# Kernel tuning notes

Measured on AMD Instinct MI355X. Metric: run time of the kernel, lower is better.

Reference implementation:

```python
import jax, jax.numpy as jnp
import numpy as np

B, N, C_IN, C_OUT, K = 2, 8192, 128, 128, 21  # K = num_neighbors + 1 (self)
EPS = 1e-5

def knn_idx(xyz, k):
    # xyz: [B,N,3] -> idx [B,N,k] of k nearest neighbors (self included)
    d2 = jnp.sum(xyz * xyz, axis=-1)  # [B,N]
    dist = d2[:, :, None] + d2[:, None, :] - 2.0 * jnp.einsum('bnd,bmd->bnm', xyz, xyz)
    _, idx = jax.lax.top_k(-dist, k)
    return idx

def group_points(pts, idx):
    # pts [B,N,D], idx [B,N,K] -> [B,N,K,D]
    return jax.vmap(lambda p, i: p[i])(pts, idx)

def group_feats(f, idx):
    # f [B,C,N], idx [B,N,K] -> [B,C,N,K]
    return jax.vmap(lambda ff, i: ff[:, i])(f, idx)

def conv_bn_relu(x, W, g, b, m, v):
    # 1x1 conv (bias=False) + BatchNorm (inference stats) + ReLU
    y = jnp.einsum('oc,bcnk->bonk', W, x)
    inv = g / jnp.sqrt(v + EPS)
    return jax.nn.relu(y * inv[None, :, None, None] + (b - m * inv)[None, :, None, None])

def setup_inputs():
    key = jax.random.key(0)
    ks = jax.random.split(key, 12)
    return {
        'xyz': jax.random.normal(ks[0], (B, N, 3), jnp.float32),
        'f': jax.random.normal(ks[1], (B, C_IN, N), jnp.float32),
        'W_geo': jax.random.normal(ks[2], (C_OUT, 6), jnp.float32) * 0.1,
        'g_geo': jax.random.uniform(ks[3], (C_OUT,), jnp.float32, 0.5, 1.5),
        'b_geo': jax.random.normal(ks[4], (C_OUT,), jnp.float32) * 0.1,
        'm_geo': jax.random.normal(ks[5], (C_OUT,), jnp.float32) * 0.1,
        'v_geo': jax.random.uniform(ks[6], (C_OUT,), jnp.float32, 0.5, 1.5),
        'W_feat': jax.random.normal(ks[7], (C_OUT, 2 * C_IN), jnp.float32) * 0.05,
        'g_feat': jax.random.uniform(ks[8], (C_OUT,), jnp.float32, 0.5, 1.5),
        'b_feat': jax.random.normal(ks[9], (C_OUT,), jnp.float32) * 0.1,
        'm_feat': jax.random.normal(ks[10], (C_OUT,), jnp.float32) * 0.1,
        'v_feat': jax.random.uniform(ks[11], (C_OUT,), jnp.float32, 0.5, 1.5),
    }

def reference(xyz, f, W_geo, g_geo, b_geo, m_geo, v_geo, W_feat, g_feat, b_feat, m_feat, v_feat):
    idx = knn_idx(xyz, K)                                   # [B,N,K]
    grouped_xyz = group_points(xyz, idx)                    # [B,N,K,3]
    xyz_diff = jnp.transpose(grouped_xyz - xyz[:, :, None, :], (0, 3, 1, 2))  # [B,3,N,K]
    center = jnp.broadcast_to(jnp.transpose(xyz, (0, 2, 1))[:, :, :, None], (B, 3, N, K))
    G_geo = jnp.concatenate([center, xyz_diff], axis=1)     # [B,6,N,K]
    grouped_f = group_feats(f, idx)                         # [B,C,N,K]
    center_f = jnp.broadcast_to(f[:, :, :, None], (B, C_IN, N, K))
    G_feat = jnp.concatenate([center_f, grouped_f - center_f], axis=1)  # [B,2C,N,K]
    G_geo = conv_bn_relu(G_geo, W_geo, g_geo, b_geo, m_geo, v_geo)      # [B,C_OUT,N,K]
    G_feat = conv_bn_relu(G_feat, W_feat, g_feat, b_feat, m_feat, v_feat)
    feature = jnp.concatenate([G_geo, G_feat], axis=1)      # [B,2*C_OUT,N,K]
    return jnp.max(feature, axis=-1)                        # [B,2*C_OUT,N]
```

## Files before the change

### kernel.cpp

```cpp
#include <hip/hip_runtime.h>

typedef unsigned int u32;
typedef unsigned long long u64;
typedef unsigned short u16;

#define DEV __device__ __forceinline__

DEV u16 f2bf(float x) {
  u32 u = __float_as_uint(x);
  u32 r = u + 0x7fffu + ((u >> 16) & 1u);
  return (u16)(r >> 16);
}
DEV float bflo(u32 d) { return __uint_as_float(d << 16); }
DEV float bfhi(u32 d) { return __uint_as_float(d & 0xffff0000u); }
DEV u64 sortable64(double f) {
  long long b = __double_as_longlong(f);
  return (u64)b ^ (u64)((b >> 63) | (long long)0x8000000000000000ll);
}
DEV double ddist(double qx, double qy, double qz, double qd2,
                 float mxf, float myf, float mzf) {
  double cx = (double)mxf, cy = (double)myf, cz = (double)mzf;
  double cd2 = cx * cx + cy * cy + cz * cz;
  double dot = cx * qx + cy * qy + cz * qz;
  return (qd2 + cd2) - 2.0 * dot;
}

#define NB 2
#define NN 8192
#define NC 128
#define KK 21
#define MARGIN 1e-3f

__global__ __launch_bounds__(1024) void k_knnprep(
    const float* __restrict__ xyz, int* __restrict__ knn,
    const float* __restrict__ Wf, const float* __restrict__ gf, const float* __restrict__ bf_,
    const float* __restrict__ mf, const float* __restrict__ vf,
    const float* __restrict__ Wg, const float* __restrict__ gg, const float* __restrict__ bg,
    const float* __restrict__ mg, const float* __restrict__ vg,
    u16* __restrict__ Wt, float* __restrict__ beta_f,
    float* __restrict__ Wgu, float* __restrict__ Wgv, float* __restrict__ beta_g) {
  __shared__ float4 sc[NN];
  __shared__ u16 ssurv[64][128];
  __shared__ u32 scnt[64];

  const int t = threadIdx.x;

  if (blockIdx.x < 32) {
    int g = (blockIdx.x << 10) + t;
    int c = g >> 8, o = g & 255;
    float val;
    if (o < 128) {
      float inv = gf[o] / sqrtf(vf[o] + 1e-5f);
      val = inv * (Wf[o * 256 + c] - Wf[o * 256 + c + 128]);
    } else {
      int o2 = o - 128;
      float inv = gf[o2] / sqrtf(vf[o2] + 1e-5f);
      val = inv * Wf[o2 * 256 + c + 128];
    }
    Wt[c * 256 + o] = f2bf(val);
    if (g < 128) {
      float inv = gf[g] / sqrtf(vf[g] + 1e-5f);
      beta_f[g] = bf_[g] - mf[g] * inv;
    } else if (g < 256) {
      int oo = g - 128;
      float invg = gg[oo] / sqrtf(vg[oo] + 1e-5f);
#pragma unroll
      for (int d = 0; d < 3; ++d) {
        Wgu[oo * 3 + d] = invg * (Wg[oo * 6 + d] - Wg[oo * 6 + 3 + d]);
        Wgv[oo * 3 + d] = invg * Wg[oo * 6 + 3 + d];
      }
      beta_g[oo] = bg[oo] - mg[oo] * invg;
    }
    return;
  }

  const int kb = blockIdx.x - 32;
  const int b = kb >> 7;
  const int n0 = (kb & 127) << 6;
  const float* X = xyz + b * (NN * 3);

  if (t < 64) scnt[t] = 0u;

  const int w = t >> 6, lane = t & 63;

  float mx[4], my[4], mz[4];
#pragma unroll
  for (int i = 0; i < 4; ++i) {
    int q = n0 + (w << 2) + i;
    mx[i] = -2.0f * X[q * 3];
    my[i] = -2.0f * X[q * 3 + 1];
    mz[i] = -2.0f * X[q * 3 + 2];
  }

#pragma unroll
  for (int k = 0; k < 8; ++k) {
    int c = (k << 10) + t;
    float x = X[c * 3], y = X[c * 3 + 1], z = X[c * 3 + 2];
    float d2 = __builtin_fmaf(x, x, __builtin_fmaf(y, y, z * z));
    sc[c] = make_float4(x, y, z, d2);
  }
  __syncthreads();

  float mn[4];
#pragma unroll
  for (int i = 0; i < 4; ++i) mn[i] = __builtin_inff();

#pragma unroll 4
  for (int cc = 0; cc < NN; cc += 64) {
    float4 C = sc[cc + lane];
#pragma unroll
    for (int i = 0; i < 4; ++i) {
      float s = __builtin_fmaf(C.x, mx[i],
                __builtin_fmaf(C.y, my[i],
                __builtin_fmaf(C.z, mz[i], C.w)));
      mn[i] = fminf(mn[i], s);
    }
  }

  float thr[4];
#pragma unroll
  for (int i = 0; i < 4; ++i) {
    float v = mn[i];
#pragma unroll
    for (int k = 2; k <= 64; k <<= 1) {
#pragma unroll
      for (int j = k >> 1; j > 0; j >>= 1) {
        float p = __shfl_xor(v, j);
        bool takeMin = (((lane & k) == 0) == ((lane & j) == 0));
        v = takeMin ? fminf(v, p) : fmaxf(v, p);
      }
    }
    thr[i] = __shfl(v, 20) + MARGIN;
  }

#pragma unroll 2
  for (int cc = 0; cc < NN; cc += 64) {
    float4 C = sc[cc + lane];
    int mbase = cc + lane;
#pragma unroll
    for (int i = 0; i < 4; ++i) {
      float s = __builtin_fmaf(C.x, mx[i],
                __builtin_fmaf(C.y, my[i],
                __builtin_fmaf(C.z, mz[i], C.w)));
      if (s <= thr[i]) {
        int qq = (w << 2) + i;
        u32 slot = atomicAdd(&scnt[qq], 1u);
        if (slot < 128u) ssurv[qq][slot] = (u16)mbase;
      }
    }
  }
  __syncthreads();

#pragma unroll 1
  for (int i = 0; i < 4; ++i) {
    const int qq = (w << 2) + i;
    const int q = n0 + qq;
    double Qx = (double)X[q * 3], Qy = (double)X[q * 3 + 1], Qz = (double)X[q * 3 + 2];
    double Qd2 = Qx * Qx + Qy * Qy + Qz * Qz;
    u32 cnt = scnt[qq];
    int* outp = knn + ((b << 13) + q) * KK;

    bool v0 = ((u32)lane < cnt);
    u32 m0 = v0 ? (u32)ssurv[qq][lane] : 0u;
    double s0 = ddist(Qx, Qy, Qz, Qd2, X[m0 * 3], X[m0 * 3 + 1], X[m0 * 3 + 2]);
    u64 k0 = v0 ? ((sortable64(s0) & 0xFFFFFFFFFFFFE000ull) | (u64)m0) : ~0ull;

    if (cnt <= 64u) {
      u64 v = k0;
#pragma unroll
      for (int k = 2; k <= 64; k <<= 1) {
#pragma unroll
        for (int j = k >> 1; j > 0; j >>= 1) {
          u64 p = __shfl_xor(v, j);
          bool takeMin = (((lane & k) == 0) == ((lane & j) == 0));
          bool pl = p < v;
          u64 mnv = pl ? p : v;
          u64 mxv = pl ? v : p;
          v = takeMin ? mnv : mxv;
        }
      }
      if (lane < KK) outp[lane] = (int)(v & 8191ull);
    } else {
      bool v1 = ((u32)(lane + 64) < cnt);
      u32 m1 = v1 ? (u32)ssurv[qq][lane + 64] : 0u;
      double s1 = ddist(Qx, Qy, Qz, Qd2, X[m1 * 3], X[m1 * 3 + 1], X[m1 * 3 + 2]);
      u64 k1 = v1 ? ((sortable64(s1) & 0xFFFFFFFFFFFFE000ull) | (u64)m1) : ~0ull;
      u32 selm = 0;
      for (int r = 0; r < KK; ++r) {
        u64 mk = (k0 < k1) ? k0 : k1;
#pragma unroll
        for (int j = 32; j > 0; j >>= 1) {
          u64 p = __shfl_xor(mk, j);
          if (p < mk) mk = p;
        }
        if (k0 == mk) k0 = ~0ull;
        else if (k1 == mk) k1 = ~0ull;
        if (lane == r) selm = (u32)(mk & 8191ull);
      }
      if (lane < KK) outp[lane] = (int)selm;
    }
  }
}

__global__ __launch_bounds__(256) void k_feat(
    const float* __restrict__ f, const u32* __restrict__ Wt32, const float* __restrict__ beta_f,
    const float* __restrict__ xyz, const float* __restrict__ Wgu, const float* __restrict__ Wgv,
    const float* __restrict__ beta_g, u32* __restrict__ ucat, u32* __restrict__ vcat) {
  __shared__ u32 sW[128 * 64];
  __shared__ float sF[128][68];

  const int t = threadIdx.x;
  const int blk = blockIdx.x;
  const int H = blk & 1;
  const int b = blk >> 8;
  const int n0 = ((blk >> 1) & 127) << 6;
  const int boff = b * (NC * NN);

#pragma unroll
  for (int k = 0; k < 32; ++k) {
    int i = t + (k << 8);
    sW[i] = Wt32[((i >> 6) << 7) + (H << 6) + (i & 63)];
  }
#pragma unroll
  for (int k = 0; k < 32; ++k) {
    int i = t + (k << 8);
    int c = i >> 6, col = i & 63;
    sF[c][col] = f[boff + c * NN + n0 + col];
  }
  __syncthreads();

  const int w = t >> 6, lane = t & 63;
  const int og = lane >> 4, pg = lane & 15;
  const int o0 = (w << 5) + (og << 3);
  const int p0 = pg << 2;

  float acc[8][4];
#pragma unroll
  for (int a = 0; a < 8; ++a)
#pragma unroll
    for (int p = 0; p < 4; ++p) acc[a][p] = 0.0f;

  for (int c = 0; c < 128; ++c) {
    float4 fa = *(const float4*)&sF[c][p0];
    uint4 wr = *(const uint4*)&sW[(c << 6) + (o0 >> 1)];
    float wv[8] = {bflo(wr.x), bfhi(wr.x), bflo(wr.y), bfhi(wr.y),
                   bflo(wr.z), bfhi(wr.z), bflo(wr.w), bfhi(wr.w)};
    float fv[4] = {fa.x, fa.y, fa.z, fa.w};
#pragma unroll
    for (int a = 0; a < 8; ++a)
#pragma unroll
      for (int p = 0; p < 4; ++p) acc[a][p] = __builtin_fmaf(wv[a], fv[p], acc[a][p]);
  }

  float bet[8];
#pragma unroll
  for (int a = 0; a < 8; ++a) bet[a] = (H == 0) ? beta_f[o0 + a] : 0.0f;
  u32* dstbase = (H == 0) ? ucat : vcat;
#pragma unroll
  for (int p = 0; p < 4; ++p) {
    int pt = (b << 13) + n0 + p0 + p;
    u32 d0 = (u32)f2bf(acc[0][p] + bet[0]) | ((u32)f2bf(acc[1][p] + bet[1]) << 16);
    u32 d1 = (u32)f2bf(acc[2][p] + bet[2]) | ((u32)f2bf(acc[3][p] + bet[3]) << 16);
    u32 d2 = (u32)f2bf(acc[4][p] + bet[4]) | ((u32)f2bf(acc[5][p] + bet[5]) << 16);
    u32 d3 = (u32)f2bf(acc[6][p] + bet[6]) | ((u32)f2bf(acc[7][p] + bet[7]) << 16);
    *(uint4*)&dstbase[pt * 128 + 64 + (o0 >> 1)] = make_uint4(d0, d1, d2, d3);
  }

  {
    const int oc = lane;
    const float* Ws = (H == 0) ? Wgu : Wgv;
    const int o0g = oc * 2, o1g = oc * 2 + 1;
    float w0x = Ws[o0g * 3], w0y = Ws[o0g * 3 + 1], w0z = Ws[o0g * 3 + 2];
    float w1x = Ws[o1g * 3], w1y = Ws[o1g * 3 + 1], w1z = Ws[o1g * 3 + 2];
    float b0 = (H == 0) ? beta_g[o0g] : 0.0f;
    float b1 = (H == 0) ? beta_g[o1g] : 0.0f;
#pragma unroll 4
    for (int j = 0; j < 16; ++j) {
      int pt = n0 + (w << 4) + j;
      const float* xp = xyz + ((b << 13) + pt) * 3;
      float X = xp[0], Y = xp[1], Z = xp[2];
      float v0 = X * w0x + Y * w0y + Z * w0z + b0;
      float v1 = X * w1x + Y * w1y + Z * w1z + b1;
      dstbase[(((b << 13) + pt) << 7) + oc] =
          (u32)f2bf(v0) | ((u32)f2bf(v1) << 16);
    }
  }
}

__global__ __launch_bounds__(256) void k_gather(
    const u32* __restrict__ ucat, const u32* __restrict__ vcat,
    const int* __restrict__ knn, float* __restrict__ out) {
  __shared__ float tr[64 * 65];

  const int t = threadIdx.x;
  const int blk = blockIdx.x;
  const int Q = blk & 3;
  const int b = blk >> 9;
  const int n0 = ((blk >> 2) & 127) << 6;
  const int w = t >> 6, lane = t & 63;
  const int half = lane >> 5;
  const int l32 = lane & 31;
  const int lo = (Q << 5) | l32;

  for (int step = 0; step < 8; ++step) {
    int qq = (step << 3) + (w << 1) + half;
    int q = n0 + qq;
    const int* ip = knn + ((b << 13) + q) * KK;
    float a0 = -__builtin_inff(), a1 = -__builtin_inff();
#pragma unroll
    for (int k = 0; k < KK; ++k) {
      int p = ip[k];
      u32 d = vcat[(((b << 13) + p) << 7) + lo];
      a0 = fmaxf(a0, bflo(d));
      a1 = fmaxf(a1, bfhi(d));
    }
    u32 u = ucat[(((b << 13) + q) << 7) + lo];
    tr[qq * 65 + l32] = fmaxf(bflo(u) + a0, 0.0f);
    tr[qq * 65 + 32 + l32] = fmaxf(bfhi(u) + a1, 0.0f);
  }
  __syncthreads();

  float* ob = out + b * (256 * NN) + (Q << 6) * NN;
  for (int i = 0; i < 16; ++i) {
    int o = (w << 4) + i;
    int col = ((o & 1) << 5) + (o >> 1);
    __builtin_nontemporal_store(tr[lane * 65 + col], &ob[o * NN + n0 + lane]);
  }
}

extern "C" void kernel_launch(void* const* d_in, const int* in_sizes, int n_in,
                              void* d_out, int out_size, void* d_ws, size_t ws_size,
                              hipStream_t stream) {
  const float* xyz = (const float*)d_in[0];
  const float* f   = (const float*)d_in[1];
  const float* Wg  = (const float*)d_in[2];
  const float* gg  = (const float*)d_in[3];
  const float* bg  = (const float*)d_in[4];
  const float* mg  = (const float*)d_in[5];
  const float* vg  = (const float*)d_in[6];
  const float* Wf  = (const float*)d_in[7];
  const float* gf  = (const float*)d_in[8];
  const float* bf_ = (const float*)d_in[9];
  const float* mf  = (const float*)d_in[10];
  const float* vf  = (const float*)d_in[11];

  char* ws = (char*)d_ws;
  u16*   Wt     = (u16*)ws;
  float* beta_f = (float*)(ws + 65536);
  float* Wgu    = (float*)(ws + 66048);
  float* Wgv    = (float*)(ws + 67584);
  float* beta_g = (float*)(ws + 69120);
  u32*   ucat   = (u32*)(ws + 69632);
  u32*   vcat   = (u32*)(ws + 69632 + 8388608);
  int*   knn    = (int*)(ws + 69632 + 2 * 8388608);
  float* out    = (float*)d_out;

  if (ws_size < (size_t)(69632 + 2 * 8388608 + 16384 * KK * 4)) return;

  k_knnprep<<<dim3(288), dim3(1024), 0, stream>>>(
      xyz, knn, Wf, gf, bf_, mf, vf, Wg, gg, bg, mg, vg,
      Wt, beta_f, Wgu, Wgv, beta_g);
  k_feat<<<dim3(512), dim3(256), 0, stream>>>(
      f, (const u32*)Wt, beta_f, xyz, Wgu, Wgv, beta_g, ucat, vcat);
  k_gather<<<dim3(1024), dim3(256), 0, stream>>>(ucat, vcat, knn, out);
}
```

Measured before the change: 174.8 us.

## Split KNN candidate scan across wave halves with packed float2 FMA

Each wave now handles 8 queries over half of the candidate set instead of 4 queries over all candidates. It uses packed two-wide FMA and min to evaluate two queries per instruction. Per-half 21st-smallest thresholds are combined through shared memory by taking their minimum, which adds a barrier. The survivor count is also clamped to 128, guarding against overflow from the looser threshold.

```diff
diff --git a/kernel.cpp b/kernel.cpp
--- a/kernel.cpp
+++ b/kernel.cpp
@@ -3,6 +3,7 @@
 typedef unsigned int u32;
 typedef unsigned long long u64;
 typedef unsigned short u16;
+typedef float v2f __attribute__((ext_vector_type(2)));
 
 #define DEV __device__ __forceinline__
 
@@ -24,6 +25,8 @@
   double dot = cx * qx + cy * qy + cz * qz;
   return (qd2 + cd2) - 2.0 * dot;
 }
+DEV v2f vfma2(v2f a, v2f b, v2f c) { return __builtin_elementwise_fma(a, b, c); }
+DEV v2f vmin2(v2f a, v2f b) { return __builtin_elementwise_min(a, b); }
 
 #define NB 2
 #define NN 8192
@@ -42,6 +45,7 @@
   __shared__ float4 sc[NN];
   __shared__ u16 ssurv[64][128];
   __shared__ u32 scnt[64];
+  __shared__ float sthr[2][64];
 
   const int t = threadIdx.x;
 
@@ -82,14 +86,19 @@
   if (t < 64) scnt[t] = 0u;
 
   const int w = t >> 6, lane = t & 63;
-
-  float mx[4], my[4], mz[4];
-#pragma unroll
-  for (int i = 0; i < 4; ++i) {
-    int q = n0 + (w << 2) + i;
-    mx[i] = -2.0f * X[q * 3];
-    my[i] = -2.0f * X[q * 3 + 1];
-    mz[i] = -2.0f * X[q * 3 + 2];
+  const int g = w & 7;
+  const int h = w >> 3;
+  const int cbase = h << 12;
+  const int q8 = n0 + (g << 3);
+
+  v2f mxp[4], myp[4], mzp[4], mnp[4];
+#pragma unroll
+  for (int j = 0; j < 4; ++j) {
+    int qa = q8 + 2 * j, qb = qa + 1;
+    mxp[j] = (v2f){-2.0f * X[qa * 3], -2.0f * X[qb * 3]};
+    myp[j] = (v2f){-2.0f * X[qa * 3 + 1], -2.0f * X[qb * 3 + 1]};
+    mzp[j] = (v2f){-2.0f * X[qa * 3 + 2], -2.0f * X[qb * 3 + 2]};
+    mnp[j] = (v2f){__builtin_inff(), __builtin_inff()};
   }
 
 #pragma unroll
@@ -101,51 +110,63 @@
   }
   __syncthreads();
 
-  float mn[4];
-#pragma unroll
-  for (int i = 0; i < 4; ++i) mn[i] = __builtin_inff();
-
 #pragma unroll 4
-  for (int cc = 0; cc < NN; cc += 64) {
-    float4 C = sc[cc + lane];
-#pragma unroll
-    for (int i = 0; i < 4; ++i) {
-      float s = __builtin_fmaf(C.x, mx[i],
-                __builtin_fmaf(C.y, my[i],
-                __builtin_fmaf(C.z, mz[i], C.w)));
-      mn[i] = fminf(mn[i], s);
-    }
-  }
-
-  float thr[4];
-#pragma unroll
-  for (int i = 0; i < 4; ++i) {
-    float v = mn[i];
-#pragma unroll
-    for (int k = 2; k <= 64; k <<= 1) {
-#pragma unroll
-      for (int j = k >> 1; j > 0; j >>= 1) {
-        float p = __shfl_xor(v, j);
-        bool takeMin = (((lane & k) == 0) == ((lane & j) == 0));
-        v = takeMin ? fminf(v, p) : fmaxf(v, p);
-      }
-    }
-    thr[i] = __shfl(v, 20) + MARGIN;
+  for (int cc = 0; cc < NN / 2; cc += 64) {
+    float4 C = sc[cbase + cc + lane];
+    v2f cx = (v2f){C.x, C.x}, cy = (v2f){C.y, C.y};
+    v2f cz = (v2f){C.z, C.z}, cw = (v2f){C.w, C.w};
+#pragma unroll
+    for (int j = 0; j < 4; ++j) {
+      v2f s = vfma2(cx, mxp[j], vfma2(cy, myp[j], vfma2(cz, mzp[j], cw)));
+      mnp[j] = vmin2(mnp[j], s);
+    }
+  }
+
+#pragma unroll
+  for (int j = 0; j < 4; ++j) {
+#pragma unroll
+    for (int e = 0; e < 2; ++e) {
+      float v = e ? mnp[j].y : mnp[j].x;
+#pragma unroll
+      for (int k = 2; k <= 64; k <<= 1) {
+#pragma unroll
+        for (int jj = k >> 1; jj > 0; jj >>= 1) {
+          float p = __shfl_xor(v, jj);
+          bool takeMin = (((lane & k) == 0) == ((lane & jj) == 0));
+          v = takeMin ? fminf(v, p) : fmaxf(v, p);
+        }
+      }
+      float tw = __shfl(v, 20);
+      if (lane == 0) sthr[h][(g << 3) + 2 * j + e] = tw;
+    }
+  }
+  __syncthreads();
+  float thr[8];
+#pragma unroll
+  for (int i = 0; i < 8; ++i) {
+    int qq = (g << 3) + i;
+    thr[i] = fminf(sthr[0][qq], sthr[1][qq]) + MARGIN;
   }
 
 #pragma unroll 2
-  for (int cc = 0; cc < NN; cc += 64) {
-    float4 C = sc[cc + lane];
-    int mbase = cc + lane;
-#pragma unroll
-    for (int i = 0; i < 4; ++i) {
-      float s = __builtin_fmaf(C.x, mx[i],
-                __builtin_fmaf(C.y, my[i],
-                __builtin_fmaf(C.z, mz[i], C.w)));
-      if (s <= thr[i]) {
-        int qq = (w << 2) + i;
-        u32 slot = atomicAdd(&scnt[qq], 1u);
-        if (slot < 128u) ssurv[qq][slot] = (u16)mbase;
+  for (int cc = 0; cc < NN / 2; cc += 64) {
+    float4 C = sc[cbase + cc + lane];
+    v2f cx = (v2f){C.x, C.x}, cy = (v2f){C.y, C.y};
+    v2f cz = (v2f){C.z, C.z}, cw = (v2f){C.w, C.w};
+    int mbase = cbase + cc + lane;
+#pragma unroll
+    for (int j = 0; j < 4; ++j) {
+      v2f s = vfma2(cx, mxp[j], vfma2(cy, myp[j], vfma2(cz, mzp[j], cw)));
+      int qa = (g << 3) + 2 * j, qb = qa + 1;
+      if (s.x <= thr[2 * j] || s.y <= thr[2 * j + 1]) {
+        if (s.x <= thr[2 * j]) {
+          u32 slot = atomicAdd(&scnt[qa], 1u);
+          if (slot < 128u) ssurv[qa][slot] = (u16)mbase;
+        }
+        if (s.y <= thr[2 * j + 1]) {
+          u32 slot = atomicAdd(&scnt[qb], 1u);
+          if (slot < 128u) ssurv[qb][slot] = (u16)mbase;
+        }
       }
     }
   }
@@ -158,6 +179,7 @@
     double Qx = (double)X[q * 3], Qy = (double)X[q * 3 + 1], Qz = (double)X[q * 3 + 2];
     double Qd2 = Qx * Qx + Qy * Qy + Qz * Qz;
     u32 cnt = scnt[qq];
+    if (cnt > 128u) cnt = 128u;
     int* outp = knn + ((b << 13) + q) * KK;
 
     bool v0 = ((u32)lane < cnt);
```

After: 181.3 us. 3.7% more time.

## Fold weight prep into KNN blocks and unroll candidate filter four-wide

Applied to the files above, without the earlier changes.

The 32 separate weight-preparation blocks are removed. Their work is spread over the first 128 threads of each of the 256 KNN blocks, which drops the extra block launch cost and the tail imbalance. The candidate filtering loop now processes four 64-point chunks per iteration, with one combined min test before the per-candidate atomic appends. This cuts branch overhead and raises ILP in the hot scan, at the cost of more registers per thread.

```diff
diff --git a/kernel.cpp b/kernel.cpp
--- a/kernel.cpp
+++ b/kernel.cpp
@@ -45,8 +45,8 @@
 
   const int t = threadIdx.x;
 
-  if (blockIdx.x < 32) {
-    int g = (blockIdx.x << 10) + t;
+  if (t < 128) {
+    int g = (blockIdx.x << 7) + t;
     int c = g >> 8, o = g & 255;
     float val;
     if (o < 128) {
@@ -71,10 +71,9 @@
       }
       beta_g[oo] = bg[oo] - mg[oo] * invg;
     }
-    return;
-  }
-
-  const int kb = blockIdx.x - 32;
+  }
+
+  const int kb = blockIdx.x;
   const int b = kb >> 7;
   const int n0 = (kb & 127) << 6;
   const float* X = xyz + b * (NN * 3);
@@ -133,19 +132,45 @@
     thr[i] = __shfl(v, 20) + MARGIN;
   }
 
-#pragma unroll 2
-  for (int cc = 0; cc < NN; cc += 64) {
-    float4 C = sc[cc + lane];
-    int mbase = cc + lane;
+#pragma unroll 1
+  for (int cc = 0; cc < NN; cc += 256) {
+    float4 C0 = sc[cc + lane];
+    float4 C1 = sc[cc + 64 + lane];
+    float4 C2 = sc[cc + 128 + lane];
+    float4 C3 = sc[cc + 192 + lane];
 #pragma unroll
     for (int i = 0; i < 4; ++i) {
-      float s = __builtin_fmaf(C.x, mx[i],
-                __builtin_fmaf(C.y, my[i],
-                __builtin_fmaf(C.z, mz[i], C.w)));
-      if (s <= thr[i]) {
+      float s0 = __builtin_fmaf(C0.x, mx[i],
+                 __builtin_fmaf(C0.y, my[i],
+                 __builtin_fmaf(C0.z, mz[i], C0.w)));
+      float s1 = __builtin_fmaf(C1.x, mx[i],
+                 __builtin_fmaf(C1.y, my[i],
+                 __builtin_fmaf(C1.z, mz[i], C1.w)));
+      float s2 = __builtin_fmaf(C2.x, mx[i],
+                 __builtin_fmaf(C2.y, my[i],
+                 __builtin_fmaf(C2.z, mz[i], C2.w)));
+      float s3 = __builtin_fmaf(C3.x, mx[i],
+                 __builtin_fmaf(C3.y, my[i],
+                 __builtin_fmaf(C3.z, mz[i], C3.w)));
+      float worst = fminf(fminf(s0, s1), fminf(s2, s3));
+      if (worst <= thr[i]) {
         int qq = (w << 2) + i;
-        u32 slot = atomicAdd(&scnt[qq], 1u);
-        if (slot < 128u) ssurv[qq][slot] = (u16)mbase;
+        if (s0 <= thr[i]) {
+          u32 slot = atomicAdd(&scnt[qq], 1u);
+          if (slot < 128u) ssurv[qq][slot] = (u16)(cc + lane);
+        }
+        if (s1 <= thr[i]) {
+          u32 slot = atomicAdd(&scnt[qq], 1u);
+          if (slot < 128u) ssurv[qq][slot] = (u16)(cc + 64 + lane);
+        }
+        if (s2 <= thr[i]) {
+          u32 slot = atomicAdd(&scnt[qq], 1u);
+          if (slot < 128u) ssurv[qq][slot] = (u16)(cc + 128 + lane);
+        }
+        if (s3 <= thr[i]) {
+          u32 slot = atomicAdd(&scnt[qq], 1u);
+          if (slot < 128u) ssurv[qq][slot] = (u16)(cc + 192 + lane);
+        }
       }
     }
   }
@@ -357,7 +382,7 @@
 
   if (ws_size < (size_t)(69632 + 2 * 8388608 + 16384 * KK * 4)) return;
 
-  k_knnprep<<<dim3(288), dim3(1024), 0, stream>>>(
+  k_knnprep<<<dim3(256), dim3(1024), 0, stream>>>(
       xyz, knn, Wf, gf, bf_, mf, vf, Wg, gg, bg, mg, vg,
       Wt, beta_f, Wgu, Wgv, beta_g);
   k_feat<<<dim3(512), dim3(256), 0, stream>>>(
```

Measured after the change: 172.5 us, median of 2. No clear change (-1.3%).

## Pack KNN distance math into float2 FMAs and fold weight prep into KNN blocks

Applied to the files above, without the earlier changes.

The KNN threshold and filter loops now compute distances for query pairs with packed two-wide FMA/min operations, which can map to packed FP32 instructions. The filter loop processes four candidate chunks per iteration and skips the per-candidate atomic path when the chunk minimum is above threshold. Weight preprocessing moves from 32 dedicated blocks into the first 128 threads of each of the 256 KNN blocks, removing the extra blocks from the grid. The risks are higher register pressure from the wider unroll and a small serial prologue added to every KNN block.

```diff
diff --git a/kernel.cpp b/kernel.cpp
--- a/kernel.cpp
+++ b/kernel.cpp
@@ -3,6 +3,7 @@
 typedef unsigned int u32;
 typedef unsigned long long u64;
 typedef unsigned short u16;
+typedef float v2f __attribute__((ext_vector_type(2)));
 
 #define DEV __device__ __forceinline__
 
@@ -24,6 +25,8 @@
   double dot = cx * qx + cy * qy + cz * qz;
   return (qd2 + cd2) - 2.0 * dot;
 }
+DEV v2f vfma2(v2f a, v2f b, v2f c) { return __builtin_elementwise_fma(a, b, c); }
+DEV v2f vmin2(v2f a, v2f b) { return __builtin_elementwise_min(a, b); }
 
 #define NB 2
 #define NN 8192
@@ -45,8 +48,8 @@
 
   const int t = threadIdx.x;
 
-  if (blockIdx.x < 32) {
-    int g = (blockIdx.x << 10) + t;
+  if (t < 128) {
+    int g = (blockIdx.x << 7) + t;
     int c = g >> 8, o = g & 255;
     float val;
     if (o < 128) {
@@ -71,10 +74,9 @@
       }
       beta_g[oo] = bg[oo] - mg[oo] * invg;
     }
-    return;
-  }
-
-  const int kb = blockIdx.x - 32;
+  }
+
+  const int kb = blockIdx.x;
   const int b = kb >> 7;
   const int n0 = (kb & 127) << 6;
   const float* X = xyz + b * (NN * 3);
@@ -91,6 +93,10 @@
     my[i] = -2.0f * X[q * 3 + 1];
     mz[i] = -2.0f * X[q * 3 + 2];
   }
+  const v2f mx01 = {mx[0], mx[1]}, my01 = {my[0], my[1]}, mz01 = {mz[0], mz[1]};
+  const v2f mx23 = {mx[2], mx[3]}, my23 = {my[2], my[3]}, mz23 = {mz[2], mz[3]};
+  v2f mn01 = {__builtin_inff(), __builtin_inff()};
+  v2f mn23 = {__builtin_inff(), __builtin_inff()};
 
 #pragma unroll
   for (int k = 0; k < 8; ++k) {
@@ -101,21 +107,16 @@
   }
   __syncthreads();
 
-  float mn[4];
-#pragma unroll
-  for (int i = 0; i < 4; ++i) mn[i] = __builtin_inff();
-
 #pragma unroll 4
   for (int cc = 0; cc < NN; cc += 64) {
     float4 C = sc[cc + lane];
-#pragma unroll
-    for (int i = 0; i < 4; ++i) {
-      float s = __builtin_fmaf(C.x, mx[i],
-                __builtin_fmaf(C.y, my[i],
-                __builtin_fmaf(C.z, mz[i], C.w)));
-      mn[i] = fminf(mn[i], s);
-    }
-  }
+    v2f cx = {C.x, C.x}, cy = {C.y, C.y}, cz = {C.z, C.z}, cw = {C.w, C.w};
+    v2f s01 = vfma2(cx, mx01, vfma2(cy, my01, vfma2(cz, mz01, cw)));
+    v2f s23 = vfma2(cx, mx23, vfma2(cy, my23, vfma2(cz, mz23, cw)));
+    mn01 = vmin2(mn01, s01);
+    mn23 = vmin2(mn23, s23);
+  }
+  float mn[4] = {mn01.x, mn01.y, mn23.x, mn23.y};
 
   float thr[4];
 #pragma unroll
@@ -133,20 +134,54 @@
     thr[i] = __shfl(v, 20) + MARGIN;
   }
 
-#pragma unroll 2
-  for (int cc = 0; cc < NN; cc += 64) {
-    float4 C = sc[cc + lane];
-    int mbase = cc + lane;
-#pragma unroll
-    for (int i = 0; i < 4; ++i) {
-      float s = __builtin_fmaf(C.x, mx[i],
-                __builtin_fmaf(C.y, my[i],
-                __builtin_fmaf(C.z, mz[i], C.w)));
-      if (s <= thr[i]) {
-        int qq = (w << 2) + i;
-        u32 slot = atomicAdd(&scnt[qq], 1u);
-        if (slot < 128u) ssurv[qq][slot] = (u16)mbase;
-      }
+#pragma unroll 1
+  for (int cc = 0; cc < NN; cc += 256) {
+    float4 C0 = sc[cc + lane];
+    float4 C1 = sc[cc + 64 + lane];
+    float4 C2 = sc[cc + 128 + lane];
+    float4 C3 = sc[cc + 192 + lane];
+    v2f c0x = {C0.x, C0.x}, c0y = {C0.y, C0.y}, c0z = {C0.z, C0.z}, c0w = {C0.w, C0.w};
+    v2f c1x = {C1.x, C1.x}, c1y = {C1.y, C1.y}, c1z = {C1.z, C1.z}, c1w = {C1.w, C1.w};
+    v2f c2x = {C2.x, C2.x}, c2y = {C2.y, C2.y}, c2z = {C2.z, C2.z}, c2w = {C2.w, C2.w};
+    v2f c3x = {C3.x, C3.x}, c3y = {C3.y, C3.y}, c3z = {C3.z, C3.z}, c3w = {C3.w, C3.w};
+    v2f s01_0 = vfma2(c0x, mx01, vfma2(c0y, my01, vfma2(c0z, mz01, c0w)));
+    v2f s01_1 = vfma2(c1x, mx01, vfma2(c1y, my01, vfma2(c1z, mz01, c1w)));
+    v2f s01_2 = vfma2(c2x, mx01, vfma2(c2y, my01, vfma2(c2z, mz01, c2w)));
+    v2f s01_3 = vfma2(c3x, mx01, vfma2(c3y, my01, vfma2(c3z, mz01, c3w)));
+    v2f s23_0 = vfma2(c0x, mx23, vfma2(c0y, my23, vfma2(c0z, mz23, c0w)));
+    v2f s23_1 = vfma2(c1x, mx23, vfma2(c1y, my23, vfma2(c1z, mz23, c1w)));
+    v2f s23_2 = vfma2(c2x, mx23, vfma2(c2y, my23, vfma2(c2z, mz23, c2w)));
+    v2f s23_3 = vfma2(c3x, mx23, vfma2(c3y, my23, vfma2(c3z, mz23, c3w)));
+    v2f w01 = vmin2(vmin2(s01_0, s01_1), vmin2(s01_2, s01_3));
+    v2f w23 = vmin2(vmin2(s23_0, s23_1), vmin2(s23_2, s23_3));
+
+    if (w01.x <= thr[0]) {
+      int qq = (w << 2);
+      if (s01_0.x <= thr[0]) { u32 s = atomicAdd(&scnt[qq], 1u); if (s < 128u) ssurv[qq][s] = (u16)(cc + lane); }
+      if (s01_1.x <= thr[0]) { u32 s = atomicAdd(&scnt[qq], 1u); if (s < 128u) ssurv[qq][s] = (u16)(cc + 64 + lane); }
+      if (s01_2.x <= thr[0]) { u32 s = atomicAdd(&scnt[qq], 1u); if (s < 128u) ssurv[qq][s] = (u16)(cc + 128 + lane); }
+      if (s01_3.x <= thr[0]) { u32 s = atomicAdd(&scnt[qq], 1u); if (s < 128u) ssurv[qq][s] = (u16)(cc + 192 + lane); }
+    }
+    if (w01.y <= thr[1]) {
+      int qq = (w << 2) + 1;
+      if (s01_0.y <= thr[1]) { u32 s = atomicAdd(&scnt[qq], 1u); if (s < 128u) ssurv[qq][s] = (u16)(cc + lane); }
+      if (s01_1.y <= thr[1]) { u32 s = atomicAdd(&scnt[qq], 1u); if (s < 128u) ssurv[qq][s] = (u16)(cc + 64 + lane); }
+      if (s01_2.y <= thr[1]) { u32 s = atomicAdd(&scnt[qq], 1u); if (s < 128u) ssurv[qq][s] = (u16)(cc + 128 + lane); }
+      if (s01_3.y <= thr[1]) { u32 s = atomicAdd(&scnt[qq], 1u); if (s < 128u) ssurv[qq][s] = (u16)(cc + 192 + lane); }
+    }
+    if (w23.x <= thr[2]) {
+      int qq = (w << 2) + 2;
+      if (s23_0.x <= thr[2]) { u32 s = atomicAdd(&scnt[qq], 1u); if (s < 128u) ssurv[qq][s] = (u16)(cc + lane); }
+      if (s23_1.x <= thr[2]) { u32 s = atomicAdd(&scnt[qq], 1u); if (s < 128u) ssurv[qq][s] = (u16)(cc + 64 + lane); }
+      if (s23_2.x <= thr[2]) { u32 s = atomicAdd(&scnt[qq], 1u); if (s < 128u) ssurv[qq][s] = (u16)(cc + 128 + lane); }
+      if (s23_3.x <= thr[2]) { u32 s = atomicAdd(&scnt[qq], 1u); if (s < 128u) ssurv[qq][s] = (u16)(cc + 192 + lane); }
+    }
+    if (w23.y <= thr[3]) {
+      int qq = (w << 2) + 3;
+      if (s23_0.y <= thr[3]) { u32 s = atomicAdd(&scnt[qq], 1u); if (s < 128u) ssurv[qq][s] = (u16)(cc + lane); }
+      if (s23_1.y <= thr[3]) { u32 s = atomicAdd(&scnt[qq], 1u); if (s < 128u) ssurv[qq][s] = (u16)(cc + 64 + lane); }
+      if (s23_2.y <= thr[3]) { u32 s = atomicAdd(&scnt[qq], 1u); if (s < 128u) ssurv[qq][s] = (u16)(cc + 128 + lane); }
+      if (s23_3.y <= thr[3]) { u32 s = atomicAdd(&scnt[qq], 1u); if (s < 128u) ssurv[qq][s] = (u16)(cc + 192 + lane); }
     }
   }
   __syncthreads();
@@ -357,7 +392,7 @@
 
   if (ws_size < (size_t)(69632 + 2 * 8388608 + 16384 * KK * 4)) return;
 
-  k_knnprep<<<dim3(288), dim3(1024), 0, stream>>>(
+  k_knnprep<<<dim3(256), dim3(1024), 0, stream>>>(
       xyz, knn, Wf, gf, bf_, mf, vf, Wg, gg, bg, mg, vg,
       Wt, beta_f, Wgu, Wgv, beta_g);
   k_feat<<<dim3(512), dim3(256), 0, stream>>>(
```

Result: no change. 177.1 us (+1.3%).
